# Performance work log

Measured on AMD Instinct MI355X. Metric: run time of the kernel, lower is better.

## Reference

```python
import jax, jax.numpy as jnp
import numpy as np

B, N, C, S = 16, 1024, 16, 8
TYPE_DIM, TOK_DIM, D, O = 128, 128, 256, 256
NUM_TYPES, NUM_TOKENS, L = 200, 50000, 2
NEG = -1000000000000.0


def setup_inputs() -> dict:
    key = jax.random.key(0)
    ks = jax.random.split(key, 8)
    node_type = jax.random.randint(ks[0], (B, N), 0, NUM_TYPES)
    node_tokens = jax.random.randint(ks[1], (B, N, S), 0, NUM_TOKENS)
    children_index = jax.random.randint(ks[2], (B, N, C), 0, N)
    # padding_idx=0 -> row 0 of both embedding tables is zero
    type_table = (0.02 * jax.random.normal(ks[3], (NUM_TYPES, TYPE_DIM))).at[0].set(0.0)
    token_table = (0.02 * jax.random.normal(ks[4], (NUM_TOKENS, TOK_DIM))).at[0].set(0.0)
    W_parent = 0.02 * jax.random.normal(ks[5], (TYPE_DIM + TOK_DIM, D))
    b_parent = jnp.zeros((D,), jnp.float32)
    conv_w = 0.02 * jax.random.normal(ks[6], (L, 3, D, O))  # stacked [w_t, w_r, w_l] per layer
    conv_b = jnp.zeros((L, O), jnp.float32)
    attn_a = 0.02 * jax.random.normal(ks[7], (O,))
    return dict(node_type=node_type, node_tokens=node_tokens, children_index=children_index,
                type_table=type_table, token_table=token_table, W_parent=W_parent,
                b_parent=b_parent, conv_w=conv_w, conv_b=conv_b, attn_a=attn_a)


def _gather_children(parent, idx):
    # parent: [B,N,Dim]; idx: [B,N,C] with 0 meaning 'no child' (zero vector)
    lookup = parent.at[:, 0, :].set(0.0)
    return jax.vmap(lambda v, i: v[i])(lookup, idx)  # [B,N,C,Dim]


def _tbcnn_coef(children):
    # Standard TBCNN positional coefficients over [parent, child_1..child_C].
    b, n, c = children.shape
    f = jnp.float32
    cmask = (children > 0).astype(f)                                      # [B,N,C]
    mask = jnp.concatenate([jnp.zeros((b, n, 1), f), cmask], axis=2)      # [B,N,C+1]
    eta_t = jnp.concatenate([jnp.ones((b, n, 1), f), jnp.zeros((b, n, c), f)], axis=2)
    num_sib = jnp.sum(cmask, axis=2, keepdims=True)                       # [B,N,1]
    pos = jnp.arange(-1.0, c, dtype=f)                                    # [-1,0,...,C-1]
    child_idx = pos[None, None, :] * mask
    singles = jnp.concatenate([jnp.zeros((b, n, 1), f), jnp.full((b, n, 1), 0.5, f),
                               jnp.zeros((b, n, c - 1), f)], axis=2)
    denom = jnp.maximum(num_sib - 1.0, 1.0)
    eta_r = jnp.where(num_sib == 1.0, singles, mask * child_idx / denom)
    eta_l = (1.0 - eta_t) * (1.0 - eta_r) * mask
    return jnp.stack([eta_t, eta_r, eta_l], axis=3)                       # [B,N,C+1,3]


def _forward(node_type, node_tokens, children_index, type_table, token_table,
             W_parent, b_parent, conv_w, conv_b, attn_a):
    # --- embeddings + parent projection ---
    type_emb = type_table[node_type]                       # [B,N,TYPE_DIM]
    tok_emb = token_table[node_tokens].sum(axis=2)         # [B,N,TOK_DIM] (sum over subtokens)
    parent = jnp.concatenate([type_emb, tok_emb], axis=-1) @ W_parent + b_parent  # [B,N,D]
    # --- tree convolutions ---
    coef = _tbcnn_coef(children_index)                     # [B,N,C+1,3]
    nodes = parent
    ch = _gather_children(nodes, children_index)           # [B,N,C,D]
    n_layers = conv_w.shape[0]
    for l in range(n_layers):
        tree = jnp.concatenate([nodes[:, :, None, :], ch], axis=2)  # [B,N,C+1,D]
        mixed = jnp.einsum('bnck,bncd->bnkd', coef, tree)           # [B,N,3,D]
        nodes = jnp.tanh(jnp.einsum('bnkd,kdo->bno', mixed, conv_w[l]) + conv_b[l])
        if l < n_layers - 1:
            ch = _gather_children(nodes, children_index)
    # --- attention aggregation ---
    m = (node_type != 0)[..., None]                        # [B,N,1] bool
    score = jnp.einsum('bno,o->bn', nodes, attn_a)[..., None]
    score = jnp.where(m, score, NEG)
    w = jax.nn.sigmoid(score)
    code_vector = jnp.mean(nodes * m * w, axis=1)          # [B,O]
    return code_vector, nodes


def reference(node_type, node_tokens, children_index, type_table, token_table,
              W_parent, b_parent, conv_w, conv_b, attn_a):
    return _forward(node_type, node_tokens, children_index, type_table, token_table,
                    W_parent, b_parent, conv_w, conv_b, attn_a)
```

## Files before the change

kernel.cpp:

```cpp
#include <hip/hip_runtime.h>
#include <math.h>

constexpr int Bsz = 16, Nn = 1024, Cc = 16, Ss = 8;
constexpr int BN = Bsz * Nn;
constexpr int EQ = 16;
constexpr int CQ = 32;

typedef __attribute__((ext_vector_type(8))) short bf16x8;
typedef __attribute__((ext_vector_type(4))) float f32x4;
typedef __attribute__((ext_vector_type(4))) unsigned short u16x4;

__device__ inline unsigned short f2bf_rne(float x) {
    unsigned u = __builtin_bit_cast(unsigned, x);
    unsigned r = (u + 0x7FFFu + ((u >> 16) & 1u)) >> 16;
    return (unsigned short)r;
}
__device__ inline float bf2f(unsigned short h) {
    unsigned u = ((unsigned)h) << 16;
    return __builtin_bit_cast(float, u);
}
__device__ inline float fast_tanh(float x) {
    const float ax = fabsf(x);
    const float t  = __expf(-2.f * ax);
    const float r  = __fdividef(1.f - t, 1.f + t);
    return copysignf(r, x);
}

__global__ __launch_bounds__(256) void pack_all_kernel(
    const float* __restrict__ conv_w,
    const float* __restrict__ Wp,
    unsigned short* __restrict__ whi, unsigned short* __restrict__ wpq)
{
    if (blockIdx.x < 192) {
        const int t = blockIdx.x * 256 + threadIdx.x;
        const int col = t & 255;
        const int gg  = (t >> 8) & 3;
        const int kb  = (t >> 10) % 24;
        const int l   = t / (24 * 4 * 256);
        const float* W = conv_w + (size_t)l * 768 * 256;
        const size_t dst = (size_t)t * 8;
        #pragma unroll
        for (int i = 0; i < 8; ++i)
            whi[dst + i] = f2bf_rne(W[(size_t)(kb * 32 + gg * 8 + i) * 256 + col]);
    } else {
        const int t = (blockIdx.x - 192) * 256 + threadIdx.x;
        const int col = t & 255;
        const int gg  = (t >> 8) & 3;
        const int kb  = t >> 10;
        const size_t dst = (size_t)t * 8;
        #pragma unroll
        for (int i = 0; i < 8; ++i)
            wpq[dst + i] = f2bf_rne(Wp[(size_t)(kb * 32 + gg * 8 + i) * 256 + col]);
    }
}

__global__ __launch_bounds__(256, 4) void emb_mfma_kernel(
    const int* __restrict__ node_type, const int* __restrict__ node_tokens,
    const float* __restrict__ type_table, const float* __restrict__ token_table,
    const unsigned short* __restrict__ wpq,
    const float* __restrict__ bp,
    unsigned short* __restrict__ outh)
{
    constexpr int AP = 264;
    __shared__ unsigned short A[EQ][AP];

    const int tid  = threadIdx.x;
    const int lane = tid & 63;
    const int w    = tid >> 6;
    const int g0   = blockIdx.x * EQ;

    #pragma unroll
    for (int it = 0; it < 4; ++it) {
        const int r = w * 4 + it;
        const int gnode = g0 + r;
        if (lane < 32) {
            const int tt = node_type[gnode];
            const float4 v = *reinterpret_cast<const float4*>(
                type_table + (size_t)tt * 128 + lane * 4);
            u16x4 s;
            s.x = f2bf_rne(v.x); s.y = f2bf_rne(v.y);
            s.z = f2bf_rne(v.z); s.w = f2bf_rne(v.w);
            *reinterpret_cast<u16x4*>(&A[r][lane * 4]) = s;
        } else {
            const int q = lane - 32;
            float4 acc = {0.f, 0.f, 0.f, 0.f};
            #pragma unroll
            for (int si = 0; si < Ss; ++si) {
                const int tok = node_tokens[gnode * Ss + si];
                const float4 v = *reinterpret_cast<const float4*>(
                    token_table + (size_t)tok * 128 + q * 4);
                acc.x += v.x; acc.y += v.y; acc.z += v.z; acc.w += v.w;
            }
            u16x4 s;
            s.x = f2bf_rne(acc.x); s.y = f2bf_rne(acc.y);
            s.z = f2bf_rne(acc.z); s.w = f2bf_rne(acc.w);
            *reinterpret_cast<u16x4*>(&A[r][128 + q * 4]) = s;
        }
    }
    __syncthreads();

    const int colg = w * 64;
    const int rr   = lane & 15;
    const int g    = lane >> 4;

    const unsigned short* pwh = wpq + ((size_t)(g * 256 + colg + rr)) * 8;

    f32x4 acc[4];
    #pragma unroll
    for (int f = 0; f < 4; ++f) acc[f] = (f32x4){0.f, 0.f, 0.f, 0.f};

    bf16x8 bA[4], bB[4];
    #pragma unroll
    for (int f = 0; f < 4; ++f)
        bA[f] = *reinterpret_cast<const bf16x8*>(pwh + f * 128);

    for (int kb = 0; kb < 8; kb += 2) {
        {
            const int o1 = (kb + 1) * 8192;
            #pragma unroll
            for (int f = 0; f < 4; ++f)
                bB[f] = *reinterpret_cast<const bf16x8*>(pwh + o1 + f * 128);
        }
        {
            const int k0 = kb * 32 + g * 8;
            const bf16x8 ah = *reinterpret_cast<const bf16x8*>(&A[rr][k0]);
            #pragma unroll
            for (int f = 0; f < 4; ++f)
                acc[f] = __builtin_amdgcn_mfma_f32_16x16x32_bf16(ah, bA[f], acc[f], 0, 0, 0);
        }
        if (kb + 2 < 8) {
            const int o2 = (kb + 2) * 8192;
            #pragma unroll
            for (int f = 0; f < 4; ++f)
                bA[f] = *reinterpret_cast<const bf16x8*>(pwh + o2 + f * 128);
        }
        {
            const int k0 = (kb + 1) * 32 + g * 8;
            const bf16x8 ah = *reinterpret_cast<const bf16x8*>(&A[rr][k0]);
            #pragma unroll
            for (int f = 0; f < 4; ++f)
                acc[f] = __builtin_amdgcn_mfma_f32_16x16x32_bf16(ah, bB[f], acc[f], 0, 0, 0);
        }
    }

    #pragma unroll
    for (int f = 0; f < 4; ++f) {
        const int col = colg + f * 16 + rr;
        const float bv = bp[col];
        #pragma unroll
        for (int i = 0; i < 4; ++i) {
            const int row = g * 4 + i;
            outh[(size_t)(g0 + row) * 256 + col] = f2bf_rne(acc[f][i] + bv);
        }
    }
}

template<int FUSE>
__global__ __launch_bounds__(512, 4) void conv_mfma_kernel(
    const unsigned short* __restrict__ in_h,
    const int* __restrict__ children_index,
    const unsigned short* __restrict__ whi,
    const float* __restrict__ bias,
    unsigned short* __restrict__ out_h,
    float* __restrict__ out_f,
    const int* __restrict__ node_type,
    const float* __restrict__ attn_a,
    float* __restrict__ partial)
{
    constexpr int AP = 776;
    __shared__ unsigned short Ahi[CQ][AP];
    __shared__ unsigned short idx_s[CQ][Cc];
    __shared__ float etar_s[CQ][Cc];
    __shared__ float etal_s[CQ][Cc];
    __shared__ float sc_lds[8][CQ];
    __shared__ float wm_lds[CQ];

    const int tid = threadIdx.x;

    const int P = blockIdx.x;
    const int xx = P & 7;
    const int rst = P >> 3;
    const int j = rst & 31;
    const int yy = rst >> 5;
    const int batch = xx + 8 * yy;
    const int g0 = batch * Nn + j * CQ;
    const unsigned short* inb = in_h + (size_t)batch * Nn * 256;

    {
        const int r = tid >> 4, c = tid & 15;
        idx_s[r][c] = (unsigned short)children_index[(size_t)(g0 + r) * Cc + c];
    }
    __syncthreads();
    {
        const int r = tid >> 4, c = tid & 15;
        int ns = 0;
        #pragma unroll
        for (int q = 0; q < Cc; ++q) ns += (idx_s[r][q] > 0) ? 1 : 0;
        const bool cm = idx_s[r][c] > 0;
        float er;
        if (ns == 1) {
            er = (c == 0) ? 0.5f : 0.f;
        } else {
            const float denom = (float)((ns - 1 > 1) ? (ns - 1) : 1);
            er = (float)c / denom;
        }
        etar_s[r][c] = cm ? er : 0.f;
        etal_s[r][c] = cm ? (1.f - er) : 0.f;
    }
    __syncthreads();

    {
        const int q = tid & 63;
        const int rgrp = tid >> 6;
        #pragma unroll
        for (int rr4 = 0; rr4 < 4; ++rr4) {
            const int r = rgrp * 4 + rr4;
            const u16x4 m0h = *reinterpret_cast<const u16x4*>(
                in_h + (size_t)(g0 + r) * 256 + q * 4);
            float4 m1 = {0.f, 0.f, 0.f, 0.f};
            float4 m2 = {0.f, 0.f, 0.f, 0.f};
            #pragma unroll
            for (int c = 0; c < Cc; ++c) {
                const int ci = idx_s[r][c];
                const u16x4 vh = *reinterpret_cast<const u16x4*>(
                    inb + (size_t)ci * 256 + q * 4);
                const float vx = bf2f(vh.x), vy = bf2f(vh.y);
                const float vz = bf2f(vh.z), vw = bf2f(vh.w);
                const float er = etar_s[r][c];
                const float el = etal_s[r][c];
                m1.x = fmaf(er, vx, m1.x); m1.y = fmaf(er, vy, m1.y);
                m1.z = fmaf(er, vz, m1.z); m1.w = fmaf(er, vw, m1.w);
                m2.x = fmaf(el, vx, m2.x); m2.y = fmaf(el, vy, m2.y);
                m2.z = fmaf(el, vz, m2.z); m2.w = fmaf(el, vw, m2.w);
            }
            u16x4 s1, s2;
            s1.x = f2bf_rne(m1.x); s1.y = f2bf_rne(m1.y);
            s1.z = f2bf_rne(m1.z); s1.w = f2bf_rne(m1.w);
            s2.x = f2bf_rne(m2.x); s2.y = f2bf_rne(m2.y);
            s2.z = f2bf_rne(m2.z); s2.w = f2bf_rne(m2.w);
            *reinterpret_cast<u16x4*>(&Ahi[r][q * 4])       = m0h;
            *reinterpret_cast<u16x4*>(&Ahi[r][256 + q * 4]) = s1;
            *reinterpret_cast<u16x4*>(&Ahi[r][512 + q * 4]) = s2;
        }
    }
    __syncthreads();

    const int lane = tid & 63;
    const int w    = tid >> 6;
    const int colg = w * 32;
    const int rr   = lane & 15;
    const int g    = lane >> 4;

    const unsigned short* pwh = whi + ((size_t)(g * 256 + colg + rr)) * 8;

    f32x4 acc[2][2];
    #pragma unroll
    for (int t = 0; t < 2; ++t)
        #pragma unroll
        for (int f = 0; f < 2; ++f) acc[t][f] = (f32x4){0.f, 0.f, 0.f, 0.f};

    bf16x8 bA[2], bB[2];
    #pragma unroll
    for (int f = 0; f < 2; ++f)
        bA[f] = *reinterpret_cast<const bf16x8*>(pwh + f * 128);

    __builtin_amdgcn_s_setprio(1);
    for (int kb = 0; kb < 24; kb += 2) {
        {
            const int o1 = (kb + 1) * 8192;
            #pragma unroll
            for (int f = 0; f < 2; ++f)
                bB[f] = *reinterpret_cast<const bf16x8*>(pwh + o1 + f * 128);
        }
        {
            const int k0 = kb * 32 + g * 8;
            const bf16x8 a0 = *reinterpret_cast<const bf16x8*>(&Ahi[rr][k0]);
            const bf16x8 a1 = *reinterpret_cast<const bf16x8*>(&Ahi[16 + rr][k0]);
            #pragma unroll
            for (int f = 0; f < 2; ++f) {
                acc[0][f] = __builtin_amdgcn_mfma_f32_16x16x32_bf16(a0, bA[f], acc[0][f], 0, 0, 0);
                acc[1][f] = __builtin_amdgcn_mfma_f32_16x16x32_bf16(a1, bA[f], acc[1][f], 0, 0, 0);
            }
        }
        if (kb + 2 < 24) {
            const int o2 = (kb + 2) * 8192;
            #pragma unroll
            for (int f = 0; f < 2; ++f)
                bA[f] = *reinterpret_cast<const bf16x8*>(pwh + o2 + f * 128);
        }
        {
            const int k0 = (kb + 1) * 32 + g * 8;
            const bf16x8 a0 = *reinterpret_cast<const bf16x8*>(&Ahi[rr][k0]);
            const bf16x8 a1 = *reinterpret_cast<const bf16x8*>(&Ahi[16 + rr][k0]);
            #pragma unroll
            for (int f = 0; f < 2; ++f) {
                acc[0][f] = __builtin_amdgcn_mfma_f32_16x16x32_bf16(a0, bB[f], acc[0][f], 0, 0, 0);
                acc[1][f] = __builtin_amdgcn_mfma_f32_16x16x32_bf16(a1, bB[f], acc[1][f], 0, 0, 0);
            }
        }
    }
    __builtin_amdgcn_s_setprio(0);

    float nd[2][2][4];
    #pragma unroll
    for (int t = 0; t < 2; ++t)
        #pragma unroll
        for (int f = 0; f < 2; ++f) {
            const int col = colg + f * 16 + rr;
            const float bv = bias[col];
            #pragma unroll
            for (int i = 0; i < 4; ++i) {
                const int row = t * 16 + g * 4 + i;
                const float v = fast_tanh(acc[t][f][i] + bv);
                nd[t][f][i] = v;
                if (FUSE) out_f[(size_t)(g0 + row) * 256 + col] = v;
                else      out_h[(size_t)(g0 + row) * 256 + col] = f2bf_rne(v);
            }
        }

    if (FUSE) {
        float av[2];
        #pragma unroll
        for (int f = 0; f < 2; ++f) av[f] = attn_a[colg + f * 16 + rr];

        float s[2][4];
        #pragma unroll
        for (int t = 0; t < 2; ++t)
            #pragma unroll
            for (int i = 0; i < 4; ++i) {
                float v = 0.f;
                #pragma unroll
                for (int f = 0; f < 2; ++f) v = fmaf(nd[t][f][i], av[f], v);
                s[t][i] = v;
            }
        #pragma unroll
        for (int off = 1; off < 16; off <<= 1)
            #pragma unroll
            for (int t = 0; t < 2; ++t)
                #pragma unroll
                for (int i = 0; i < 4; ++i)
                    s[t][i] += __shfl_xor(s[t][i], off, 64);
        if (rr == 0) {
            #pragma unroll
            for (int t = 0; t < 2; ++t)
                #pragma unroll
                for (int i = 0; i < 4; ++i)
                    sc_lds[w][t * 16 + g * 4 + i] = s[t][i];
        }
        __syncthreads();
        if (tid < CQ) {
            float sc = 0.f;
            #pragma unroll
            for (int ww = 0; ww < 8; ++ww) sc += sc_lds[ww][tid];
            float wmv = 0.f;
            if (node_type[g0 + tid] != 0)
                wmv = __fdividef(1.f, 1.f + __expf(-sc));
            wm_lds[tid] = wmv;
        }
        __syncthreads();

        float qf[2];
        #pragma unroll
        for (int f = 0; f < 2; ++f) {
            float v = 0.f;
            #pragma unroll
            for (int t = 0; t < 2; ++t)
                #pragma unroll
                for (int i = 0; i < 4; ++i)
                    v = fmaf(wm_lds[t * 16 + g * 4 + i], nd[t][f][i], v);
            qf[f] = v;
        }
        #pragma unroll
        for (int f = 0; f < 2; ++f) {
            qf[f] += __shfl_xor(qf[f], 16, 64);
            qf[f] += __shfl_xor(qf[f], 32, 64);
        }
        if (g == 0) {
            const int pidx = batch * 32 + j;
            #pragma unroll
            for (int f = 0; f < 2; ++f)
                partial[(size_t)pidx * 256 + colg + f * 16 + rr] = qf[f];
        }
    }
}

__global__ __launch_bounds__(256) void final_kernel(
    const float* __restrict__ partial, float* __restrict__ code)
{
    const int i = blockIdx.x * 256 + threadIdx.x;
    const int b = i >> 8, o = i & 255;
    float acc = 0.f;
    #pragma unroll
    for (int c = 0; c < 32; ++c) acc += partial[(size_t)(b * 32 + c) * 256 + o];
    code[i] = acc * (1.f / 1024.f);
}

extern "C" void kernel_launch(void* const* d_in, const int* in_sizes, int n_in,
                              void* d_out, int out_size, void* d_ws, size_t ws_size,
                              hipStream_t stream)
{
    const int*   node_type   = (const int*)d_in[0];
    const int*   node_tokens = (const int*)d_in[1];
    const int*   children    = (const int*)d_in[2];
    const float* type_table  = (const float*)d_in[3];
    const float* token_table = (const float*)d_in[4];
    const float* Wp          = (const float*)d_in[5];
    const float* bp          = (const float*)d_in[6];
    const float* conv_w      = (const float*)d_in[7];
    const float* conv_b      = (const float*)d_in[8];
    const float* attn_a      = (const float*)d_in[9];

    float* out    = (float*)d_out;
    float* code   = out;
    float* nodesF = out + 4096;

    unsigned short* nodes0 = (unsigned short*)d_ws;
    unsigned short* nodes1 = nodes0 + (size_t)BN * 256;
    float* partial = (float*)(nodes1 + (size_t)BN * 256);
    unsigned short* whi = (unsigned short*)(partial + 512 * 256);
    unsigned short* wpq = whi + 2 * 196608;

    constexpr int LSTRIDE = 196608;

    pack_all_kernel<<<224, 256, 0, stream>>>(conv_w, Wp, whi, wpq);

    emb_mfma_kernel<<<BN / EQ, 256, 0, stream>>>(
        node_type, node_tokens, type_table, token_table, wpq, bp, nodes0);

    conv_mfma_kernel<0><<<BN / CQ, 512, 0, stream>>>(
        nodes0, children, whi, conv_b, nodes1,
        nullptr, nullptr, nullptr, nullptr);

    conv_mfma_kernel<1><<<BN / CQ, 512, 0, stream>>>(
        nodes1, children, whi + LSTRIDE, conv_b + 256, nullptr,
        nodesF, node_type, attn_a, partial);

    final_kernel<<<16, 256, 0, stream>>>(partial, code);
}
```

Before: 70.73 us.

## Fuse conv weight packing into embedding kernel and final reduction into last conv

Conv weight packing now runs in the first 192 blocks of the embedding kernel after their MFMA work, so only the small Wp pack stays a separate launch. The final per-batch mean is folded into the last conv kernel: an atomic counter per batch picks the last-finishing block, which sums the partials. The token-embedding gather is split across both half-waves with a shuffle-add. These changes cut kernel launches and serial dependencies, but add a memset, a threadfence and atomics, plus extra tail work in some embedding blocks.

```diff
diff --git a/kernel.cpp b/kernel.cpp
--- a/kernel.cpp
+++ b/kernel.cpp
@@ -26,13 +26,131 @@
     return copysignf(r, x);
 }
 
-__global__ __launch_bounds__(256) void pack_all_kernel(
+__global__ __launch_bounds__(256) void pack_wp_kernel(
+    const float* __restrict__ Wp, unsigned short* __restrict__ wpq)
+{
+    const int t = blockIdx.x * 256 + threadIdx.x;
+    const int col = t & 255;
+    const int gg  = (t >> 8) & 3;
+    const int kb  = t >> 10;
+    const size_t dst = (size_t)t * 8;
+    #pragma unroll
+    for (int i = 0; i < 8; ++i)
+        wpq[dst + i] = f2bf_rne(Wp[(size_t)(kb * 32 + gg * 8 + i) * 256 + col]);
+}
+
+__global__ __launch_bounds__(256, 4) void emb_mfma_kernel(
+    const int* __restrict__ node_type, const int* __restrict__ node_tokens,
+    const float* __restrict__ type_table, const float* __restrict__ token_table,
+    const unsigned short* __restrict__ wpq,
+    const float* __restrict__ bp,
+    unsigned short* __restrict__ outh,
     const float* __restrict__ conv_w,
-    const float* __restrict__ Wp,
-    unsigned short* __restrict__ whi, unsigned short* __restrict__ wpq)
+    unsigned short* __restrict__ whi)
 {
+    constexpr int AP = 264;
+    __shared__ unsigned short A[EQ][AP];
+
+    const int tid  = threadIdx.x;
+    const int lane = tid & 63;
+    const int w    = tid >> 6;
+    const int g0   = blockIdx.x * EQ;
+
+    {
+        const int q    = lane & 31;
+        const int half = lane >> 5;
+        #pragma unroll
+        for (int it = 0; it < 4; ++it) {
+            const int r = w * 4 + it;
+            const int gnode = g0 + r;
+            f32x4 acc = (f32x4){0.f, 0.f, 0.f, 0.f};
+            #pragma unroll
+            for (int s = 0; s < 4; ++s) {
+                const int tok = node_tokens[gnode * Ss + half * 4 + s];
+                const f32x4 v = *reinterpret_cast<const f32x4*>(
+                    token_table + (size_t)tok * 128 + q * 4);
+                acc += v;
+            }
+            f32x4 tot;
+            tot.x = acc.x + __shfl_xor(acc.x, 32);
+            tot.y = acc.y + __shfl_xor(acc.y, 32);
+            tot.z = acc.z + __shfl_xor(acc.z, 32);
+            tot.w = acc.w + __shfl_xor(acc.w, 32);
+            if (half == 0) {
+                const int tt = node_type[gnode];
+                const f32x4 tv = *reinterpret_cast<const f32x4*>(
+                    type_table + (size_t)tt * 128 + q * 4);
+                u16x4 s0;
+                s0.x = f2bf_rne(tv.x); s0.y = f2bf_rne(tv.y);
+                s0.z = f2bf_rne(tv.z); s0.w = f2bf_rne(tv.w);
+                *reinterpret_cast<u16x4*>(&A[r][q * 4]) = s0;
+            } else {
+                u16x4 s1;
+                s1.x = f2bf_rne(tot.x); s1.y = f2bf_rne(tot.y);
+                s1.z = f2bf_rne(tot.z); s1.w = f2bf_rne(tot.w);
+                *reinterpret_cast<u16x4*>(&A[r][128 + q * 4]) = s1;
+            }
+        }
+    }
+    __syncthreads();
+
+    const int colg = w * 64;
+    const int rr   = lane & 15;
+    const int g    = lane >> 4;
+
+    const unsigned short* pwh = wpq + ((size_t)(g * 256 + colg + rr)) * 8;
+
+    f32x4 acc[4];
+    #pragma unroll
+    for (int f = 0; f < 4; ++f) acc[f] = (f32x4){0.f, 0.f, 0.f, 0.f};
+
+    bf16x8 bA[4], bB[4];
+    #pragma unroll
+    for (int f = 0; f < 4; ++f)
+        bA[f] = *reinterpret_cast<const bf16x8*>(pwh + f * 128);
+
+    for (int kb = 0; kb < 8; kb += 2) {
+        {
+            const int o1 = (kb + 1) * 8192;
+            #pragma unroll
+            for (int f = 0; f < 4; ++f)
+                bB[f] = *reinterpret_cast<const bf16x8*>(pwh + o1 + f * 128);
+        }
+        {
+            const int k0 = kb * 32 + g * 8;
+            const bf16x8 ah = *reinterpret_cast<const bf16x8*>(&A[rr][k0]);
+            #pragma unroll
+            for (int f = 0; f < 4; ++f)
+                acc[f] = __builtin_amdgcn_mfma_f32_16x16x32_bf16(ah, bA[f], acc[f], 0, 0, 0);
+        }
+        if (kb + 2 < 8) {
+            const int o2 = (kb + 2) * 8192;
+            #pragma unroll
+            for (int f = 0; f < 4; ++f)
+                bA[f] = *reinterpret_cast<const bf16x8*>(pwh + o2 + f * 128);
+        }
+        {
+            const int k0 = (kb + 1) * 32 + g * 8;
+            const bf16x8 ah = *reinterpret_cast<const bf16x8*>(&A[rr][k0]);
+            #pragma unroll
+            for (int f = 0; f < 4; ++f)
+                acc[f] = __builtin_amdgcn_mfma_f32_16x16x32_bf16(ah, bB[f], acc[f], 0, 0, 0);
+        }
+    }
+
+    #pragma unroll
+    for (int f = 0; f < 4; ++f) {
+        const int col = colg + f * 16 + rr;
+        const float bv = bp[col];
+        #pragma unroll
+        for (int i = 0; i < 4; ++i) {
+            const int row = g * 4 + i;
+            outh[(size_t)(g0 + row) * 256 + col] = f2bf_rne(acc[f][i] + bv);
+        }
+    }
+
     if (blockIdx.x < 192) {
-        const int t = blockIdx.x * 256 + threadIdx.x;
+        const int t = blockIdx.x * 256 + tid;
         const int col = t & 255;
         const int gg  = (t >> 8) & 3;
         const int kb  = (t >> 10) % 24;
@@ -42,116 +160,6 @@
         #pragma unroll
         for (int i = 0; i < 8; ++i)
             whi[dst + i] = f2bf_rne(W[(size_t)(kb * 32 + gg * 8 + i) * 256 + col]);
-    } else {
-        const int t = (blockIdx.x - 192) * 256 + threadIdx.x;
-        const int col = t & 255;
-        const int gg  = (t >> 8) & 3;
-        const int kb  = t >> 10;
-        const size_t dst = (size_t)t * 8;
-        #pragma unroll
-        for (int i = 0; i < 8; ++i)
-            wpq[dst + i] = f2bf_rne(Wp[(size_t)(kb * 32 + gg * 8 + i) * 256 + col]);
-    }
-}
-
-__global__ __launch_bounds__(256, 4) void emb_mfma_kernel(
-    const int* __restrict__ node_type, const int* __restrict__ node_tokens,
-    const float* __restrict__ type_table, const float* __restrict__ token_table,
-    const unsigned short* __restrict__ wpq,
-    const float* __restrict__ bp,
-    unsigned short* __restrict__ outh)
-{
-    constexpr int AP = 264;
-    __shared__ unsigned short A[EQ][AP];
-
-    const int tid  = threadIdx.x;
-    const int lane = tid & 63;
-    const int w    = tid >> 6;
-    const int g0   = blockIdx.x * EQ;
-
-    #pragma unroll
-    for (int it = 0; it < 4; ++it) {
-        const int r = w * 4 + it;
-        const int gnode = g0 + r;
-        if (lane < 32) {
-            const int tt = node_type[gnode];
-            const float4 v = *reinterpret_cast<const float4*>(
-                type_table + (size_t)tt * 128 + lane * 4);
-            u16x4 s;
-            s.x = f2bf_rne(v.x); s.y = f2bf_rne(v.y);
-            s.z = f2bf_rne(v.z); s.w = f2bf_rne(v.w);
-            *reinterpret_cast<u16x4*>(&A[r][lane * 4]) = s;
-        } else {
-            const int q = lane - 32;
-            float4 acc = {0.f, 0.f, 0.f, 0.f};
-            #pragma unroll
-            for (int si = 0; si < Ss; ++si) {
-                const int tok = node_tokens[gnode * Ss + si];
-                const float4 v = *reinterpret_cast<const float4*>(
-                    token_table + (size_t)tok * 128 + q * 4);
-                acc.x += v.x; acc.y += v.y; acc.z += v.z; acc.w += v.w;
-            }
-            u16x4 s;
-            s.x = f2bf_rne(acc.x); s.y = f2bf_rne(acc.y);
-            s.z = f2bf_rne(acc.z); s.w = f2bf_rne(acc.w);
-            *reinterpret_cast<u16x4*>(&A[r][128 + q * 4]) = s;
-        }
-    }
-    __syncthreads();
-
-    const int colg = w * 64;
-    const int rr   = lane & 15;
-    const int g    = lane >> 4;
-
-    const unsigned short* pwh = wpq + ((size_t)(g * 256 + colg + rr)) * 8;
-
-    f32x4 acc[4];
-    #pragma unroll
-    for (int f = 0; f < 4; ++f) acc[f] = (f32x4){0.f, 0.f, 0.f, 0.f};
-
-    bf16x8 bA[4], bB[4];
-    #pragma unroll
-    for (int f = 0; f < 4; ++f)
-        bA[f] = *reinterpret_cast<const bf16x8*>(pwh + f * 128);
-
-    for (int kb = 0; kb < 8; kb += 2) {
-        {
-            const int o1 = (kb + 1) * 8192;
-            #pragma unroll
-            for (int f = 0; f < 4; ++f)
-                bB[f] = *reinterpret_cast<const bf16x8*>(pwh + o1 + f * 128);
-        }
-        {
-            const int k0 = kb * 32 + g * 8;
-            const bf16x8 ah = *reinterpret_cast<const bf16x8*>(&A[rr][k0]);
-            #pragma unroll
-            for (int f = 0; f < 4; ++f)
-                acc[f] = __builtin_amdgcn_mfma_f32_16x16x32_bf16(ah, bA[f], acc[f], 0, 0, 0);
-        }
-        if (kb + 2 < 8) {
-            const int o2 = (kb + 2) * 8192;
-            #pragma unroll
-            for (int f = 0; f < 4; ++f)
-                bA[f] = *reinterpret_cast<const bf16x8*>(pwh + o2 + f * 128);
-        }
-        {
-            const int k0 = (kb + 1) * 32 + g * 8;
-            const bf16x8 ah = *reinterpret_cast<const bf16x8*>(&A[rr][k0]);
-            #pragma unroll
-            for (int f = 0; f < 4; ++f)
-                acc[f] = __builtin_amdgcn_mfma_f32_16x16x32_bf16(ah, bB[f], acc[f], 0, 0, 0);
-        }
-    }
-
-    #pragma unroll
-    for (int f = 0; f < 4; ++f) {
-        const int col = colg + f * 16 + rr;
-        const float bv = bp[col];
-        #pragma unroll
-        for (int i = 0; i < 4; ++i) {
-            const int row = g * 4 + i;
-            outh[(size_t)(g0 + row) * 256 + col] = f2bf_rne(acc[f][i] + bv);
-        }
     }
 }
 
@@ -165,15 +173,15 @@
     float* __restrict__ out_f,
     const int* __restrict__ node_type,
     const float* __restrict__ attn_a,
-    float* __restrict__ partial)
+    float* __restrict__ partial,
+    float* __restrict__ code,
+    int* __restrict__ cnt)
 {
     constexpr int AP = 776;
     __shared__ unsigned short Ahi[CQ][AP];
     __shared__ unsigned short idx_s[CQ][Cc];
     __shared__ float etar_s[CQ][Cc];
     __shared__ float etal_s[CQ][Cc];
-    __shared__ float sc_lds[8][CQ];
-    __shared__ float wm_lds[CQ];
 
     const int tid = threadIdx.x;
 
@@ -217,21 +225,18 @@
             const int r = rgrp * 4 + rr4;
             const u16x4 m0h = *reinterpret_cast<const u16x4*>(
                 in_h + (size_t)(g0 + r) * 256 + q * 4);
-            float4 m1 = {0.f, 0.f, 0.f, 0.f};
-            float4 m2 = {0.f, 0.f, 0.f, 0.f};
+            f32x4 m1 = (f32x4){0.f, 0.f, 0.f, 0.f};
+            f32x4 m2 = (f32x4){0.f, 0.f, 0.f, 0.f};
             #pragma unroll
             for (int c = 0; c < Cc; ++c) {
                 const int ci = idx_s[r][c];
                 const u16x4 vh = *reinterpret_cast<const u16x4*>(
                     inb + (size_t)ci * 256 + q * 4);
-                const float vx = bf2f(vh.x), vy = bf2f(vh.y);
-                const float vz = bf2f(vh.z), vw = bf2f(vh.w);
-                const float er = etar_s[r][c];
-                const float el = etal_s[r][c];
-                m1.x = fmaf(er, vx, m1.x); m1.y = fmaf(er, vy, m1.y);
-                m1.z = fmaf(er, vz, m1.z); m1.w = fmaf(er, vw, m1.w);
-                m2.x = fmaf(el, vx, m2.x); m2.y = fmaf(el, vy, m2.y);
-                m2.z = fmaf(el, vz, m2.z); m2.w = fmaf(el, vw, m2.w);
+                f32x4 vf;
+                vf.x = bf2f(vh.x); vf.y = bf2f(vh.y);
+                vf.z = bf2f(vh.z); vf.w = bf2f(vh.w);
+                m1 += etar_s[r][c] * vf;
+                m2 += etal_s[r][c] * vf;
             }
             u16x4 s1, s2;
             s1.x = f2bf_rne(m1.x); s1.y = f2bf_rne(m1.y);
@@ -318,7 +323,12 @@
             }
         }
 
-    if (FUSE) {
+    if constexpr (FUSE) {
+        __shared__ float sc_lds[8][CQ];
+        __shared__ float wm_lds[CQ];
+        __shared__ int   win_s;
+        __shared__ float red_s[2][256];
+
         float av[2];
         #pragma unroll
         for (int f = 0; f < 2; ++f) av[f] = attn_a[colg + f * 16 + rr];
@@ -381,18 +391,31 @@
             for (int f = 0; f < 2; ++f)
                 partial[(size_t)pidx * 256 + colg + f * 16 + rr] = qf[f];
         }
-    }
-}
-
-__global__ __launch_bounds__(256) void final_kernel(
-    const float* __restrict__ partial, float* __restrict__ code)
-{
-    const int i = blockIdx.x * 256 + threadIdx.x;
-    const int b = i >> 8, o = i & 255;
-    float acc = 0.f;
-    #pragma unroll
-    for (int c = 0; c < 32; ++c) acc += partial[(size_t)(b * 32 + c) * 256 + o];
-    code[i] = acc * (1.f / 1024.f);
+
+        __threadfence();
+        __syncthreads();
+        if (tid == 0) {
+            const int old = __hip_atomic_fetch_add(&cnt[batch], 1,
+                                __ATOMIC_ACQ_REL, __HIP_MEMORY_SCOPE_AGENT);
+            win_s = (old == 31);
+        }
+        __syncthreads();
+        if (win_s) {
+            const int o  = tid & 255;
+            const int hh = tid >> 8;
+            float a2 = 0.f;
+            #pragma unroll
+            for (int c = 0; c < 16; ++c) {
+                const int rowp = batch * 32 + hh * 16 + c;
+                a2 += __hip_atomic_load(&partial[(size_t)rowp * 256 + o],
+                                        __ATOMIC_RELAXED, __HIP_MEMORY_SCOPE_AGENT);
+            }
+            red_s[hh][o] = a2;
+            __syncthreads();
+            if (tid < 256)
+                code[batch * 256 + tid] = (red_s[0][tid] + red_s[1][tid]) * (1.f / 1024.f);
+        }
+    }
 }
 
 extern "C" void kernel_launch(void* const* d_in, const int* in_sizes, int n_in,
@@ -419,21 +442,23 @@
     float* partial = (float*)(nodes1 + (size_t)BN * 256);
     unsigned short* whi = (unsigned short*)(partial + 512 * 256);
     unsigned short* wpq = whi + 2 * 196608;
+    int* cnt = (int*)(wpq + 65536);
 
     constexpr int LSTRIDE = 196608;
 
-    pack_all_kernel<<<224, 256, 0, stream>>>(conv_w, Wp, whi, wpq);
+    hipMemsetAsync(cnt, 0, 16 * sizeof(int), stream);
+
+    pack_wp_kernel<<<32, 256, 0, stream>>>(Wp, wpq);
 
     emb_mfma_kernel<<<BN / EQ, 256, 0, stream>>>(
-        node_type, node_tokens, type_table, token_table, wpq, bp, nodes0);
+        node_type, node_tokens, type_table, token_table, wpq, bp, nodes0,
+        conv_w, whi);
 
     conv_mfma_kernel<0><<<BN / CQ, 512, 0, stream>>>(
         nodes0, children, whi, conv_b, nodes1,
-        nullptr, nullptr, nullptr, nullptr);
+        nullptr, nullptr, nullptr, nullptr, nullptr, nullptr);
 
     conv_mfma_kernel<1><<<BN / CQ, 512, 0, stream>>>(
         nodes1, children, whi + LSTRIDE, conv_b + 256, nullptr,
-        nodesF, node_type, attn_a, partial);
-
-    final_kernel<<<16, 256, 0, stream>>>(partial, code);
-}
+        nodesF, node_type, attn_a, partial, code, cnt);
+}
```

Result: slower. 150.5 us (+112.7%).
